# Kernel tuning notes

Measured on AMD Instinct MI355X. Metric: run time of the kernel, lower is better.

## Reference

```python
import jax, jax.numpy as jnp
import numpy as np

D_MODEL = 1024
NUM_HEADS = 16
D_K = D_MODEL // NUM_HEADS  # 64
MAX_SEQ_LEN = 2048
THETA = 10000.0
BATCH = 2
SEQ = 2048


def _rope_tables():
    # freqs: [d_k/2], positions: [max_seq_len] -> angles [max_seq_len, d_k/2]
    freqs = THETA ** (-jnp.arange(0, D_K, 2, dtype=jnp.float32) / D_K)
    positions = jnp.arange(MAX_SEQ_LEN, dtype=jnp.float32)[:, None]
    angles = positions * freqs[None, :]
    return jnp.cos(angles), jnp.sin(angles)


def _apply_rope(x, token_positions, cos_cached, sin_cached):
    # x: [..., seq, d_k]; token_positions: [seq]
    cos = cos_cached[token_positions]  # [seq, d_k/2]
    sin = sin_cached[token_positions]
    x_even = x[..., ::2]
    x_odd = x[..., 1::2]
    r_even = x_even * cos - x_odd * sin
    r_odd = x_even * sin + x_odd * cos
    # interleave even/odd back into last dim
    out = jnp.stack([r_even, r_odd], axis=-1)
    return out.reshape(x.shape)


def setup_inputs() -> dict:
    key = jax.random.key(0)
    ks = jax.random.split(key, 5)
    scale = 1.0 / np.sqrt(D_MODEL)
    in_features = jax.random.normal(ks[0], (BATCH, SEQ, D_MODEL), dtype=jnp.float32)
    q_proj = jax.random.normal(ks[1], (D_MODEL, D_MODEL), dtype=jnp.float32) * scale
    k_proj = jax.random.normal(ks[2], (D_MODEL, D_MODEL), dtype=jnp.float32) * scale
    v_proj = jax.random.normal(ks[3], (D_MODEL, D_MODEL), dtype=jnp.float32) * scale
    o_proj = jax.random.normal(ks[4], (D_MODEL, D_MODEL), dtype=jnp.float32) * scale
    mask = jnp.tril(jnp.ones((SEQ, SEQ), dtype=bool))  # causal
    token_positions = jnp.arange(SEQ, dtype=jnp.int32)
    return {
        "in_features": in_features,
        "q_proj": q_proj,
        "k_proj": k_proj,
        "v_proj": v_proj,
        "o_proj": o_proj,
        "mask": mask,
        "token_positions": token_positions,
    }


def reference(in_features, q_proj, k_proj, v_proj, o_proj, mask, token_positions):
    B, S, _ = in_features.shape
    cos_cached, sin_cached = _rope_tables()
    # fused QKV projection (same math as x @ cat(Wq,Wk,Wv).T then chunk)
    q = jnp.einsum("bsd,ed->bse", in_features, q_proj)
    k = jnp.einsum("bsd,ed->bse", in_features, k_proj)
    v = jnp.einsum("bsd,ed->bse", in_features, v_proj)
    # ... seq (h d) -> ... h seq d
    q = q.reshape(B, S, NUM_HEADS, D_K).transpose(0, 2, 1, 3)
    k = k.reshape(B, S, NUM_HEADS, D_K).transpose(0, 2, 1, 3)
    v = v.reshape(B, S, NUM_HEADS, D_K).transpose(0, 2, 1, 3)
    q = _apply_rope(q, token_positions, cos_cached, sin_cached)
    k = _apply_rope(k, token_positions, cos_cached, sin_cached)
    scores = jnp.einsum("bhqd,bhkd->bhqk", q, k) / np.sqrt(D_K)
    scores = jnp.where(mask, scores, -jnp.inf)
    attn = jax.nn.softmax(scores, axis=-1)
    out = jnp.einsum("bhqk,bhkd->bhqd", attn, v)
    # ... h seq d -> ... seq (h d)
    concat = out.transpose(0, 2, 1, 3).reshape(B, S, D_MODEL)
    return jnp.einsum("bsd,ed->bse", concat, o_proj)
```

## Files before the change

### kernel.cpp

```cpp
#include <hip/hip_runtime.h>
#include <cstdint>

#define D_MODEL 1024
#define NHEADS 16
#define DKH 64
#define SEQL 2048
#define NBATCH 2
#define NROWS (NBATCH * SEQL)

typedef __bf16 bf16;
typedef __bf16 bf16x2 __attribute__((ext_vector_type(2)));
typedef __bf16 bf16x4 __attribute__((ext_vector_type(4)));
typedef __bf16 bf16x8 __attribute__((ext_vector_type(8)));
typedef float f32x4 __attribute__((ext_vector_type(4)));
typedef float f32x16 __attribute__((ext_vector_type(16)));
typedef unsigned u32x4 __attribute__((ext_vector_type(4)));

static __device__ __forceinline__ f32x4 mfma16(bf16x8 a, bf16x8 b, f32x4 c) {
  return __builtin_amdgcn_mfma_f32_16x16x32_bf16(a, b, c, 0, 0, 0);
}

static __device__ __forceinline__ f32x16 mfma32(bf16x8 a, bf16x8 b, f32x16 c) {
  return __builtin_amdgcn_mfma_f32_32x32x16_bf16(a, b, c, 0, 0, 0);
}

static __device__ __forceinline__ void gload_lds16(const bf16* g, bf16* l) {
  __builtin_amdgcn_global_load_lds(
      (const __attribute__((address_space(1))) void*)g,
      (__attribute__((address_space(3))) void*)l, 16, 0, 0);
}

static __device__ __forceinline__ float fexp2(float x) {
  return __builtin_amdgcn_exp2f(x);
}

static __device__ __forceinline__ unsigned cvt_pk(float a, float b) {
  unsigned r;
  asm("v_cvt_pk_bf16_f32 %0, %1, %2" : "=v"(r) : "v"(a), "v"(b));
  return r;
}

static __device__ __forceinline__ void plswap(unsigned& a, unsigned& b) {
  asm("v_permlane32_swap_b32 %0, %1" : "+v"(a), "+v"(b));
}

__global__ __launch_bounds__(256) void convert_kernel(
    const float* __restrict__ x, const float* __restrict__ wq,
    const float* __restrict__ wk, const float* __restrict__ wv,
    const float* __restrict__ wo, bf16* __restrict__ xb,
    bf16* __restrict__ wqb, bf16* __restrict__ wkb, bf16* __restrict__ wvb,
    bf16* __restrict__ wob) {
  int i4 = blockIdx.x * 256 + threadIdx.x;
  const float* src;
  bf16* dst;
  int off;
  if (i4 < (NROWS * D_MODEL / 4)) {
    src = x; dst = xb; off = i4;
  } else {
    int j = i4 - NROWS * D_MODEL / 4;
    int sel = j >> 18;
    off = j & ((1 << 18) - 1);
    src = sel == 0 ? wq : sel == 1 ? wk : sel == 2 ? wv : wo;
    dst = sel == 0 ? wqb : sel == 1 ? wkb : sel == 2 ? wvb : wob;
  }
  float4 v = ((const float4*)src)[off];
  bf16x4 o;
  o[0] = (bf16)v.x; o[1] = (bf16)v.y; o[2] = (bf16)v.z; o[3] = (bf16)v.w;
  ((bf16x4*)dst)[off] = o;
}

__global__ __launch_bounds__(256, 3) void qkv_gemm(
    const bf16* __restrict__ A, const bf16* __restrict__ Bq,
    const bf16* __restrict__ Bk, const bf16* __restrict__ Bv,
    const int* __restrict__ tpos, bf16* __restrict__ Qb,
    bf16* __restrict__ Kb, bf16* __restrict__ Vt) {
  __shared__ bf16 As[128 * 64];
  __shared__ bf16 Bs[3][64 * 64];
  const int t = threadIdx.x, wave = t >> 6, lane = t & 63;
  const int quad = lane >> 4, l16 = lane & 15;
  const int bm = blockIdx.x * 128, bn = blockIdx.y * 64;

  f32x4 acc[3][2][4];
  for (int o = 0; o < 3; o++)
    for (int mt = 0; mt < 2; mt++)
      for (int nt = 0; nt < 4; nt++)
        for (int r = 0; r < 4; r++) acc[o][mt][nt][r] = 0.0f;

  for (int k0 = 0; k0 < D_MODEL; k0 += 64) {
    for (int j = 0; j < 4; j++) {
      int s = (wave * 4 + j) * 64 + lane;
      int srow = s >> 3, scol = (s & 7) ^ (srow & 7);
      gload_lds16(&A[(size_t)(bm + srow) * D_MODEL + k0 + scol * 8],
                  &As[(wave * 4 + j) * 512]);
    }
    for (int j = 0; j < 2; j++) {
      int s = (wave * 2 + j) * 64 + lane;
      int srow = s >> 3, scol = (s & 7) ^ (srow & 7);
      size_t goff = (size_t)(bn + srow) * D_MODEL + k0 + scol * 8;
      gload_lds16(&Bq[goff], &Bs[0][(wave * 2 + j) * 512]);
      gload_lds16(&Bk[goff], &Bs[1][(wave * 2 + j) * 512]);
      gload_lds16(&Bv[goff], &Bs[2][(wave * 2 + j) * 512]);
    }
    __syncthreads();
    for (int kh = 0; kh < 2; kh++) {
      const int kc = kh * 4 + quad;
      bf16x8 af[2];
      for (int mt = 0; mt < 2; mt++) {
        int row = wave * 32 + mt * 16 + l16;
        af[mt] = *(bf16x8*)&As[row * 64 + (kc ^ (row & 7)) * 8];
      }
      for (int nt = 0; nt < 4; nt++) {
        int row = nt * 16 + l16;
        int off = row * 64 + (kc ^ (row & 7)) * 8;
        bf16x8 bq = *(bf16x8*)&Bs[0][off];
        bf16x8 bk = *(bf16x8*)&Bs[1][off];
        bf16x8 bv = *(bf16x8*)&Bs[2][off];
        for (int mt = 0; mt < 2; mt++) {
          acc[0][mt][nt] = mfma16(af[mt], bq, acc[0][mt][nt]);
          acc[1][mt][nt] = mfma16(af[mt], bk, acc[1][mt][nt]);
          acc[2][mt][nt] = mfma16(af[mt], bv, acc[2][mt][nt]);
        }
      }
    }
    __syncthreads();
  }

  const float qsc = 0.125f * 1.44269504f;
  float freqv[4], sgn[4];
  for (int nt = 0; nt < 4; nt++) {
    int cp = (bn + nt * 16 + l16) & 63;
    freqv[nt] = fexp2((float)(cp >> 1) * -0.41524101f);
    sgn[nt] = (cp & 1) ? 1.0f : -1.0f;
  }
  for (int mt = 0; mt < 2; mt++) {
    int row0 = bm + wave * 32 + mt * 16 + quad * 4;
    for (int r = 0; r < 4; r++) {
      int row = row0 + r;
      float pos = (float)tpos[row & (SEQL - 1)];
      for (int nt = 0; nt < 4; nt++) {
        int col = bn + nt * 16 + l16;
        float sn, cs;
        __sincosf(pos * freqv[nt], &sn, &cs);
        float vq = acc[0][mt][nt][r];
        float vk = acc[1][mt][nt][r];
        float pq = __shfl_xor(vq, 1);
        float pk = __shfl_xor(vk, 1);
        float rq = vq * cs + sgn[nt] * pq * sn;
        float rk = vk * cs + sgn[nt] * pk * sn;
        Qb[(size_t)row * D_MODEL + col] = (bf16)(rq * qsc);
        Kb[(size_t)row * D_MODEL + col] = (bf16)rk;
      }
    }
    for (int nt = 0; nt < 4; nt++) {
      int col = bn + nt * 16 + l16;
      bf16x4 pv;
      for (int r = 0; r < 4; r++) pv[r] = (bf16)acc[2][mt][nt][r];
      *(bf16x4*)&Vt[(size_t)col * NROWS + row0] = pv;
    }
  }
}

__global__ __launch_bounds__(256, 3) void o_gemm(const bf16* __restrict__ A,
                                                 const bf16* __restrict__ Bm,
                                                 float* __restrict__ C) {
  constexpr int BM = 64, BN = 128, MT = 2, NT = 4, CA = 2, CB = 4;
  const int K = D_MODEL, N = D_MODEL;
  const int bm = blockIdx.x * BM, bn = blockIdx.y * BN;
  __shared__ bf16 As[2][BM * 64];
  __shared__ bf16 Bs[2][BN * 64];
  const int t = threadIdx.x;
  const int wave = t >> 6, lane = t & 63;
  const int quad = lane >> 4, l16 = lane & 15;
  const int wm = (wave >> 1) * (MT * 16), wn = (wave & 1) * (NT * 16);

  f32x4 acc[MT][NT];
  for (int i = 0; i < MT; i++)
    for (int j = 0; j < NT; j++)
      for (int r = 0; r < 4; r++) acc[i][j][r] = 0.0f;

  auto stage = [&](int buf, int k0) {
#pragma unroll
    for (int j = 0; j < CA; j++) {
      int s = (wave * CA + j) * 64 + lane;
      int srow = s >> 3, scol = (s & 7) ^ (srow & 7);
      gload_lds16(&A[(size_t)(bm + srow) * K + k0 + scol * 8],
                  &As[buf][(wave * CA + j) * 512]);
    }
#pragma unroll
    for (int j = 0; j < CB; j++) {
      int s = (wave * CB + j) * 64 + lane;
      int srow = s >> 3, scol = (s & 7) ^ (srow & 7);
      gload_lds16(&Bm[(size_t)(bn + srow) * K + k0 + scol * 8],
                  &Bs[buf][(wave * CB + j) * 512]);
    }
  };

  stage(0, 0);
  int cur = 0;
  for (int kt = 0; kt < K / 64; kt++) {
    if (kt + 1 < K / 64) {
      stage(cur ^ 1, (kt + 1) * 64);
      asm volatile("s_waitcnt vmcnt(6)" ::: "memory");
    } else {
      asm volatile("s_waitcnt vmcnt(0)" ::: "memory");
    }
    __builtin_amdgcn_sched_barrier(0);
    __builtin_amdgcn_s_barrier();

#pragma unroll
    for (int kh = 0; kh < 2; kh++) {
      const int kc = kh * 4 + quad;
      bf16x8 af[MT], bfr[NT];
#pragma unroll
      for (int mt = 0; mt < MT; mt++) {
        int row = wm + mt * 16 + l16;
        af[mt] = *(bf16x8*)&As[cur][row * 64 + (kc ^ (row & 7)) * 8];
      }
#pragma unroll
      for (int nt = 0; nt < NT; nt++) {
        int row = wn + nt * 16 + l16;
        bfr[nt] = *(bf16x8*)&Bs[cur][row * 64 + (kc ^ (row & 7)) * 8];
      }
#pragma unroll
      for (int mt = 0; mt < MT; mt++)
#pragma unroll
        for (int nt = 0; nt < NT; nt++)
          acc[mt][nt] = mfma16(af[mt], bfr[nt], acc[mt][nt]);
    }
    asm volatile("" ::: "memory");
    __builtin_amdgcn_sched_barrier(0);
    __builtin_amdgcn_s_barrier();
    cur ^= 1;
  }
  for (int mt = 0; mt < MT; mt++)
    for (int nt = 0; nt < NT; nt++)
      for (int r = 0; r < 4; r++) {
        int row = bm + wm + mt * 16 + quad * 4 + r;
        int col = bn + wn + nt * 16 + l16;
        C[(size_t)row * N + col] = acc[mt][nt][r];
      }
}

__global__ __launch_bounds__(256) void attn_kernel(
    const bf16* __restrict__ Q, const bf16* __restrict__ K,
    const bf16* __restrict__ Vt_g, float* __restrict__ O0,
    float* __restrict__ O1, float* __restrict__ O2, float* __restrict__ O3,
    float* __restrict__ L0, float* __restrict__ L1, float* __restrict__ L2,
    float* __restrict__ L3) {
  const int t = threadIdx.x;
  const int wave = t >> 6, lane = t & 63;
  const int l32 = lane & 31, hi = lane >> 5;

  const int id = blockIdx.x;
  const int bh = id & 31;
  const int c = 39 - (id >> 5);
  int qt, piece, np;
  if (c < 4)       { qt = c;                 piece = 0;            np = 1; }
  else if (c < 12) { int e = c - 4;  qt = 4 + (e >> 1); piece = e & 1; np = 2; }
  else if (c < 24) { int e = c - 12; qt = 8 + e / 3;    piece = e % 3; np = 3; }
  else             { int e = c - 24; qt = 12 + (e >> 2); piece = e & 3; np = 4; }
  const int total = qt + 1, bas = total / np, rem = total % np;
  const int len = bas + (piece < rem ? 1 : 0);
  const int k0 = piece * bas + (piece < rem ? piece : rem);

  const int b = bh >> 4, h = bh & 15;
  const int q_base = qt * 128;
  const size_t base = (size_t)b * SEQL * D_MODEL + h * DKH;

  __shared__ bf16 lds[16384];

  const int r8 = lane >> 3, c8 = lane & 7;

  for (int i = 0; i < 4; i++) {
    int row = wave * 32 + i * 8 + r8;
    int sc = c8 ^ (row & 7);
    gload_lds16(&Q[base + (size_t)(q_base + row) * D_MODEL + sc * 8],
                &lds[(wave * 32 + i * 8) * 64]);
  }
  __syncthreads();
  bf16x8 qb[4];
  {
    int row = wave * 32 + l32;
#pragma unroll
    for (int ks = 0; ks < 4; ks++) {
      int ch = (ks * 2 + hi) ^ (row & 7);
      qb[ks] = *(bf16x8*)&lds[row * 64 + ch * 8];
    }
  }
  __syncthreads();

  f32x16 oaccT[2];
  float lsum = 0.0f;
#pragma unroll
  for (int dt = 0; dt < 2; dt++)
#pragma unroll
    for (int r = 0; r < 16; r++) oaccT[dt][r] = 0.0f;

  const bf16* Vrow0 = &Vt_g[(size_t)(h * 64) * NROWS + b * SEQL];
  const int q_glob = q_base + wave * 32 + l32;

  auto stage = [&](int hc) {
    int buf = hc & 1;
    int kb = k0 * 128 + hc * 64;
#pragma unroll
    for (int i = 0; i < 2; i++) {
      int seg = wave * 2 + i;
      int row = seg * 8 + r8;
      int sc = c8 ^ (row & 7);
      gload_lds16(&K[base + (size_t)(kb + row) * D_MODEL + sc * 8],
                  &lds[buf * 4096 + seg * 512]);
      gload_lds16(&Vrow0[(size_t)row * NROWS + kb + sc * 8],
                  &lds[8192 + buf * 4096 + seg * 512]);
    }
  };

  const int nch = 2 * len;
  stage(0);
  for (int hc = 0; hc < nch; hc++) {
    if (hc + 1 < nch) {
      stage(hc + 1);
      asm volatile("s_waitcnt vmcnt(4)" ::: "memory");
    } else {
      asm volatile("s_waitcnt vmcnt(0)" ::: "memory");
    }
    __builtin_amdgcn_sched_barrier(0);
    __builtin_amdgcn_s_barrier();

    const int buf = hc & 1;
    const bf16* Kb_ = &lds[buf * 4096];
    const bf16* Vb_ = &lds[8192 + buf * 4096];
    const int kb = k0 * 128 + hc * 64;
    const bool diag = ((kb >> 7) == qt);

#pragma unroll
    for (int cc = 0; cc < 2; cc++) {
      f32x16 sT;
#pragma unroll
      for (int r = 0; r < 16; r++) sT[r] = 0.0f;
      {
        int krow = cc * 32 + l32;
        __builtin_amdgcn_s_setprio(1);
#pragma unroll
        for (int ks = 0; ks < 4; ks++) {
          int ch = (ks * 2 + hi) ^ (krow & 7);
          bf16x8 kf = *(bf16x8*)&Kb_[krow * 64 + ch * 8];
          sT = mfma32(kf, qb[ks], sT);
        }
        __builtin_amdgcn_s_setprio(0);
      }
      if (diag) {
#pragma unroll
        for (int r = 0; r < 16; r++) {
          int key = kb + cc * 32 + (r & 3) + 8 * (r >> 2) + 4 * hi;
          if (key > q_glob) sT[r] = -1e30f;
        }
      }
      float p[16];
#pragma unroll
      for (int r = 0; r < 16; r++) p[r] = fexp2(sT[r]);
      lsum += (((p[0] + p[1]) + (p[2] + p[3])) +
               ((p[4] + p[5]) + (p[6] + p[7]))) +
              (((p[8] + p[9]) + (p[10] + p[11])) +
               ((p[12] + p[13]) + (p[14] + p[15])));
      unsigned a0 = cvt_pk(p[0], p[1]),  a1 = cvt_pk(p[2], p[3]);
      unsigned b0 = cvt_pk(p[4], p[5]),  b1 = cvt_pk(p[6], p[7]);
      unsigned c0 = cvt_pk(p[8], p[9]),  c1 = cvt_pk(p[10], p[11]);
      unsigned d0 = cvt_pk(p[12], p[13]), d1 = cvt_pk(p[14], p[15]);
      plswap(a0, b0); plswap(a1, b1); plswap(c0, d0); plswap(c1, d1);
      bf16x8 pf[2];
      {
        u32x4 u = {a0, a1, b0, b1};
        pf[0] = __builtin_bit_cast(bf16x8, u);
      }
      {
        u32x4 u = {c0, c1, d0, d1};
        pf[1] = __builtin_bit_cast(bf16x8, u);
      }
      __builtin_amdgcn_s_setprio(1);
#pragma unroll
      for (int dt = 0; dt < 2; dt++) {
        int d = dt * 32 + l32;
#pragma unroll
        for (int ks = 0; ks < 2; ks++) {
          int ch = (cc * 4 + ks * 2 + hi) ^ (d & 7);
          bf16x8 vf = *(bf16x8*)&Vb_[d * 64 + ch * 8];
          oaccT[dt] = mfma32(vf, pf[ks], oaccT[dt]);
        }
      }
      __builtin_amdgcn_s_setprio(0);
    }
    asm volatile("" ::: "memory");
    __builtin_amdgcn_sched_barrier(0);
    __builtin_amdgcn_s_barrier();
  }

  lsum += __shfl_xor(lsum, 32);
  float* Ob;
  float* Lb;
  int rbase, roff;
  if (piece == 0)      { Ob = O0; Lb = L0; rbase = SEQL;        roff = 0; }
  else if (piece == 1) { Ob = O1; Lb = L1; rbase = SEQL - 512;  roff = 512; }
  else if (piece == 2) { Ob = O2; Lb = L2; rbase = SEQL - 1024; roff = 1024; }
  else                 { Ob = O3; Lb = L3; rbase = SEQL - 1536; roff = 1536; }
  {
    int qrow = q_base + wave * 32 + l32;
    size_t orow = (size_t)b * rbase + (qrow - roff);
    if (hi == 0) Lb[orow * NHEADS + h] = lsum;
#pragma unroll
    for (int dt = 0; dt < 2; dt++)
#pragma unroll
      for (int rq = 0; rq < 4; rq++) {
        f32x4 vv = {oaccT[dt][rq * 4 + 0], oaccT[dt][rq * 4 + 1],
                    oaccT[dt][rq * 4 + 2], oaccT[dt][rq * 4 + 3]};
        *(f32x4*)&Ob[orow * D_MODEL + h * DKH + dt * 32 + rq * 8 + hi * 4] =
            vv;
      }
  }
}

__global__ __launch_bounds__(256) void normalize_kernel(
    const float* __restrict__ O0, const float* __restrict__ O1,
    const float* __restrict__ O2, const float* __restrict__ O3,
    const float* __restrict__ L0, const float* __restrict__ L1,
    const float* __restrict__ L2, const float* __restrict__ L3,
    bf16* __restrict__ Cc) {
  int i4 = blockIdx.x * 256 + threadIdx.x;
  int row = i4 >> 8;
  int c0 = (i4 & 255) * 4;
  int s = row & (SEQL - 1);
  int b = row >> 11;
  int h = c0 >> 6;
  float l = L0[(size_t)row * NHEADS + h];
  f32x4 v = *(const f32x4*)&O0[(size_t)row * D_MODEL + c0];
  if (s >= 512) {
    size_t r1 = (size_t)b * (SEQL - 512) + (s - 512);
    l += L1[r1 * NHEADS + h];
    f32x4 u = *(const f32x4*)&O1[r1 * D_MODEL + c0];
    for (int r = 0; r < 4; r++) v[r] += u[r];
  }
  if (s >= 1024) {
    size_t r2 = (size_t)b * (SEQL - 1024) + (s - 1024);
    l += L2[r2 * NHEADS + h];
    f32x4 u = *(const f32x4*)&O2[r2 * D_MODEL + c0];
    for (int r = 0; r < 4; r++) v[r] += u[r];
  }
  if (s >= 1536) {
    size_t r3 = (size_t)b * (SEQL - 1536) + (s - 1536);
    l += L3[r3 * NHEADS + h];
    f32x4 u = *(const f32x4*)&O3[r3 * D_MODEL + c0];
    for (int r = 0; r < 4; r++) v[r] += u[r];
  }
  float inv = 1.0f / l;
  bf16x4 o;
  o[0] = (bf16)(v[0] * inv);
  o[1] = (bf16)(v[1] * inv);
  o[2] = (bf16)(v[2] * inv);
  o[3] = (bf16)(v[3] * inv);
  *(bf16x4*)&Cc[(size_t)row * D_MODEL + c0] = o;
}

extern "C" void kernel_launch(void* const* d_in, const int* in_sizes, int n_in,
                              void* d_out, int out_size, void* d_ws,
                              size_t ws_size, hipStream_t stream) {
  const float* x = (const float*)d_in[0];
  const float* wq = (const float*)d_in[1];
  const float* wk = (const float*)d_in[2];
  const float* wv = (const float*)d_in[3];
  const float* wo = (const float*)d_in[4];
  const int* tpos = (const int*)d_in[6];
  float* out = (float*)d_out;

  char* p = (char*)d_ws;
  bf16* xb  = (bf16*)p; p += (size_t)NROWS * D_MODEL * 2;
  bf16* wqb = (bf16*)p; p += (size_t)D_MODEL * D_MODEL * 2;
  bf16* wkb = (bf16*)p; p += (size_t)D_MODEL * D_MODEL * 2;
  bf16* wvb = (bf16*)p; p += (size_t)D_MODEL * D_MODEL * 2;
  bf16* wob = (bf16*)p; p += (size_t)D_MODEL * D_MODEL * 2;
  bf16* Qb  = (bf16*)p; p += (size_t)NROWS * D_MODEL * 2;
  bf16* Kb  = (bf16*)p; p += (size_t)NROWS * D_MODEL * 2;
  bf16* Vt  = (bf16*)p; p += (size_t)NROWS * D_MODEL * 2;
  bf16* Cc  = (bf16*)p; p += (size_t)NROWS * D_MODEL * 2;
  float* O0 = (float*)p; p += (size_t)NROWS * D_MODEL * 4;
  float* L0 = (float*)p; p += (size_t)NROWS * NHEADS * 4;
  float* O1 = (float*)p; p += (size_t)NBATCH * (SEQL - 512) * D_MODEL * 4;
  float* L1 = (float*)p; p += (size_t)NBATCH * (SEQL - 512) * NHEADS * 4;
  float* O2 = (float*)xb;
  float* O3 = (float*)wqb;
  float* L2 = (float*)wvb;
  float* L3 = (float*)wvb + (size_t)NBATCH * (SEQL - 1024) * NHEADS;

  convert_kernel<<<8192, 256, 0, stream>>>(x, wq, wk, wv, wo, xb, wqb, wkb,
                                           wvb, wob);
  qkv_gemm<<<dim3(NROWS / 128, D_MODEL / 64), 256, 0, stream>>>(
      xb, wqb, wkb, wvb, tpos, Qb, Kb, Vt);
  attn_kernel<<<1280, 256, 0, stream>>>(Qb, Kb, Vt, O0, O1, O2, O3, L0, L1,
                                        L2, L3);
  normalize_kernel<<<NROWS * D_MODEL / 1024, 256, 0, stream>>>(
      O0, O1, O2, O3, L0, L1, L2, L3, Cc);
  o_gemm<<<dim3(NROWS / 64, D_MODEL / 128), 256, 0, stream>>>(Cc, wob, out);
}
```

Before: 181.7 us.

## Fuse fp32-to-bf16 conversion into GEMM tile loads and drop convert kernel

```diff
diff --git a/kernel.cpp b/kernel.cpp
--- a/kernel.cpp
+++ b/kernel.cpp
@@ -44,34 +44,19 @@
   asm("v_permlane32_swap_b32 %0, %1" : "+v"(a), "+v"(b));
 }
 
-__global__ __launch_bounds__(256) void convert_kernel(
-    const float* __restrict__ x, const float* __restrict__ wq,
-    const float* __restrict__ wk, const float* __restrict__ wv,
-    const float* __restrict__ wo, bf16* __restrict__ xb,
-    bf16* __restrict__ wqb, bf16* __restrict__ wkb, bf16* __restrict__ wvb,
-    bf16* __restrict__ wob) {
-  int i4 = blockIdx.x * 256 + threadIdx.x;
-  const float* src;
-  bf16* dst;
-  int off;
-  if (i4 < (NROWS * D_MODEL / 4)) {
-    src = x; dst = xb; off = i4;
-  } else {
-    int j = i4 - NROWS * D_MODEL / 4;
-    int sel = j >> 18;
-    off = j & ((1 << 18) - 1);
-    src = sel == 0 ? wq : sel == 1 ? wk : sel == 2 ? wv : wo;
-    dst = sel == 0 ? wqb : sel == 1 ? wkb : sel == 2 ? wvb : wob;
-  }
-  float4 v = ((const float4*)src)[off];
-  bf16x4 o;
-  o[0] = (bf16)v.x; o[1] = (bf16)v.y; o[2] = (bf16)v.z; o[3] = (bf16)v.w;
-  ((bf16x4*)dst)[off] = o;
+static __device__ __forceinline__ void cvt16(const float* __restrict__ g,
+                                             bf16* __restrict__ l) {
+  float4 lo = ((const float4*)g)[0];
+  float4 hi = ((const float4*)g)[1];
+  bf16x8 o;
+  o[0] = (bf16)lo.x; o[1] = (bf16)lo.y; o[2] = (bf16)lo.z; o[3] = (bf16)lo.w;
+  o[4] = (bf16)hi.x; o[5] = (bf16)hi.y; o[6] = (bf16)hi.z; o[7] = (bf16)hi.w;
+  *(bf16x8*)l = o;
 }
 
 __global__ __launch_bounds__(256, 3) void qkv_gemm(
-    const bf16* __restrict__ A, const bf16* __restrict__ Bq,
-    const bf16* __restrict__ Bk, const bf16* __restrict__ Bv,
+    const float* __restrict__ A, const float* __restrict__ Bq,
+    const float* __restrict__ Bk, const float* __restrict__ Bv,
     const int* __restrict__ tpos, bf16* __restrict__ Qb,
     bf16* __restrict__ Kb, bf16* __restrict__ Vt) {
   __shared__ bf16 As[128 * 64];
@@ -90,16 +75,17 @@
     for (int j = 0; j < 4; j++) {
       int s = (wave * 4 + j) * 64 + lane;
       int srow = s >> 3, scol = (s & 7) ^ (srow & 7);
-      gload_lds16(&A[(size_t)(bm + srow) * D_MODEL + k0 + scol * 8],
-                  &As[(wave * 4 + j) * 512]);
+      cvt16(&A[(size_t)(bm + srow) * D_MODEL + k0 + scol * 8],
+            &As[(wave * 4 + j) * 512 + lane * 8]);
     }
     for (int j = 0; j < 2; j++) {
       int s = (wave * 2 + j) * 64 + lane;
       int srow = s >> 3, scol = (s & 7) ^ (srow & 7);
       size_t goff = (size_t)(bn + srow) * D_MODEL + k0 + scol * 8;
-      gload_lds16(&Bq[goff], &Bs[0][(wave * 2 + j) * 512]);
-      gload_lds16(&Bk[goff], &Bs[1][(wave * 2 + j) * 512]);
-      gload_lds16(&Bv[goff], &Bs[2][(wave * 2 + j) * 512]);
+      int loff = (wave * 2 + j) * 512 + lane * 8;
+      cvt16(&Bq[goff], &Bs[0][loff]);
+      cvt16(&Bk[goff], &Bs[1][loff]);
+      cvt16(&Bv[goff], &Bs[2][loff]);
     }
     __syncthreads();
     for (int kh = 0; kh < 2; kh++) {
@@ -161,13 +147,13 @@
 }
 
 __global__ __launch_bounds__(256, 3) void o_gemm(const bf16* __restrict__ A,
-                                                 const bf16* __restrict__ Bm,
+                                                 const float* __restrict__ Bm,
                                                  float* __restrict__ C) {
-  constexpr int BM = 64, BN = 128, MT = 2, NT = 4, CA = 2, CB = 4;
+  constexpr int MT = 2, NT = 4, CA = 2, CB = 4;
   const int K = D_MODEL, N = D_MODEL;
-  const int bm = blockIdx.x * BM, bn = blockIdx.y * BN;
-  __shared__ bf16 As[2][BM * 64];
-  __shared__ bf16 Bs[2][BN * 64];
+  const int bm = blockIdx.x * 64, bn = blockIdx.y * 128;
+  __shared__ bf16 As[64 * 64];
+  __shared__ bf16 Bs[128 * 64];
   const int t = threadIdx.x;
   const int wave = t >> 6, lane = t & 63;
   const int quad = lane >> 4, l16 = lane & 15;
@@ -178,35 +164,24 @@
     for (int j = 0; j < NT; j++)
       for (int r = 0; r < 4; r++) acc[i][j][r] = 0.0f;
 
-  auto stage = [&](int buf, int k0) {
+  for (int kt = 0; kt < K / 64; kt++) {
+    __syncthreads();
+    const int k0 = kt * 64;
 #pragma unroll
     for (int j = 0; j < CA; j++) {
       int s = (wave * CA + j) * 64 + lane;
       int srow = s >> 3, scol = (s & 7) ^ (srow & 7);
       gload_lds16(&A[(size_t)(bm + srow) * K + k0 + scol * 8],
-                  &As[buf][(wave * CA + j) * 512]);
+                  &As[(wave * CA + j) * 512]);
     }
 #pragma unroll
     for (int j = 0; j < CB; j++) {
       int s = (wave * CB + j) * 64 + lane;
       int srow = s >> 3, scol = (s & 7) ^ (srow & 7);
-      gload_lds16(&Bm[(size_t)(bn + srow) * K + k0 + scol * 8],
-                  &Bs[buf][(wave * CB + j) * 512]);
-    }
-  };
-
-  stage(0, 0);
-  int cur = 0;
-  for (int kt = 0; kt < K / 64; kt++) {
-    if (kt + 1 < K / 64) {
-      stage(cur ^ 1, (kt + 1) * 64);
-      asm volatile("s_waitcnt vmcnt(6)" ::: "memory");
-    } else {
-      asm volatile("s_waitcnt vmcnt(0)" ::: "memory");
-    }
-    __builtin_amdgcn_sched_barrier(0);
-    __builtin_amdgcn_s_barrier();
-
+      cvt16(&Bm[(size_t)(bn + srow) * K + k0 + scol * 8],
+            &Bs[(wave * CB + j) * 512 + lane * 8]);
+    }
+    __syncthreads();
 #pragma unroll
     for (int kh = 0; kh < 2; kh++) {
       const int kc = kh * 4 + quad;
@@ -214,12 +189,12 @@
 #pragma unroll
       for (int mt = 0; mt < MT; mt++) {
         int row = wm + mt * 16 + l16;
-        af[mt] = *(bf16x8*)&As[cur][row * 64 + (kc ^ (row & 7)) * 8];
+        af[mt] = *(bf16x8*)&As[row * 64 + (kc ^ (row & 7)) * 8];
       }
 #pragma unroll
       for (int nt = 0; nt < NT; nt++) {
         int row = wn + nt * 16 + l16;
-        bfr[nt] = *(bf16x8*)&Bs[cur][row * 64 + (kc ^ (row & 7)) * 8];
+        bfr[nt] = *(bf16x8*)&Bs[row * 64 + (kc ^ (row & 7)) * 8];
       }
 #pragma unroll
       for (int mt = 0; mt < MT; mt++)
@@ -227,10 +202,6 @@
         for (int nt = 0; nt < NT; nt++)
           acc[mt][nt] = mfma16(af[mt], bfr[nt], acc[mt][nt]);
     }
-    asm volatile("" ::: "memory");
-    __builtin_amdgcn_sched_barrier(0);
-    __builtin_amdgcn_s_barrier();
-    cur ^= 1;
   }
   for (int mt = 0; mt < MT; mt++)
     for (int nt = 0; nt < NT; nt++)
@@ -488,14 +459,13 @@
   float* O3 = (float*)wqb;
   float* L2 = (float*)wvb;
   float* L3 = (float*)wvb + (size_t)NBATCH * (SEQL - 1024) * NHEADS;
-
-  convert_kernel<<<8192, 256, 0, stream>>>(x, wq, wk, wv, wo, xb, wqb, wkb,
-                                           wvb, wob);
+  (void)wkb; (void)wob;
+
   qkv_gemm<<<dim3(NROWS / 128, D_MODEL / 64), 256, 0, stream>>>(
-      xb, wqb, wkb, wvb, tpos, Qb, Kb, Vt);
+      x, wq, wk, wv, tpos, Qb, Kb, Vt);
   attn_kernel<<<1280, 256, 0, stream>>>(Qb, Kb, Vt, O0, O1, O2, O3, L0, L1,
                                         L2, L3);
   normalize_kernel<<<NROWS * D_MODEL / 1024, 256, 0, stream>>>(
       O0, O1, O2, O3, L0, L1, L2, L3, Cc);
-  o_gemm<<<dim3(NROWS / 64, D_MODEL / 128), 256, 0, stream>>>(Cc, wob, out);
-}
+  o_gemm<<<dim3(NROWS / 64, D_MODEL / 128), 256, 0, stream>>>(Cc, wo, out);
+}
```

Result: slower. 224.1 us (+23.3%).
